# Kernel tuning notes

Hardware: AMD Instinct MI355X
Metric: run time of the kernel (lower is better)

The kernel has to match this reference:

```python
import jax, jax.numpy as jnp
import numpy as np

HEAD_SIZE = 64
NUM_HEADS = 8
D_MODEL = NUM_HEADS * HEAD_SIZE  # 512
B, T = 8, 1024
LN_EPS = 1e-3  # tf.keras LayerNormalization default epsilon


def setup_inputs() -> dict:
    key = jax.random.key(0)
    ks = jax.random.split(key, 10)
    s = 0.02
    return {
        "inputs": jax.random.normal(ks[0], (B, T, D_MODEL), jnp.float32),
        "pos": jax.random.normal(ks[1], (B, T, D_MODEL), jnp.float32),
        "gamma": jnp.ones((D_MODEL,), jnp.float32),
        "beta": jnp.zeros((D_MODEL,), jnp.float32),
        "query_kernel": jax.random.normal(ks[2], (NUM_HEADS, D_MODEL, HEAD_SIZE), jnp.float32) * s,
        "key_kernel": jax.random.normal(ks[3], (NUM_HEADS, D_MODEL, HEAD_SIZE), jnp.float32) * s,
        "value_kernel": jax.random.normal(ks[4], (NUM_HEADS, D_MODEL, HEAD_SIZE), jnp.float32) * s,
        "pos_kernel": jax.random.normal(ks[5], (NUM_HEADS, D_MODEL, HEAD_SIZE), jnp.float32) * s,
        "pos_bias_u": jax.random.normal(ks[6], (NUM_HEADS, HEAD_SIZE), jnp.float32) * s,
        "pos_bias_v": jax.random.normal(ks[7], (NUM_HEADS, HEAD_SIZE), jnp.float32) * s,
        "projection_kernel": jax.random.normal(ks[8], (NUM_HEADS, HEAD_SIZE, D_MODEL), jnp.float32) * s,
        "projection_bias": jnp.zeros((D_MODEL,), jnp.float32),
    }


def _layer_norm(x, gamma, beta):
    mean = jnp.mean(x, axis=-1, keepdims=True)
    var = jnp.mean(jnp.square(x - mean), axis=-1, keepdims=True)
    return (x - mean) * jax.lax.rsqrt(var + LN_EPS) * gamma + beta


def _relative_shift(x):
    # Transformer-XL shift trick: x is [B, H, N, M]
    b, h, n, m = x.shape
    x = jnp.pad(x, ((0, 0), (0, 0), (0, 0), (1, 0)))  # [B,H,N,M+1]
    x = x.reshape(b, h, m + 1, n)
    return x[:, :, 1:, :].reshape(b, h, n, m)


def reference(inputs, pos, gamma, beta, query_kernel, key_kernel, value_kernel,
              pos_kernel, pos_bias_u, pos_bias_v, projection_kernel, projection_bias):
    x = _layer_norm(inputs, gamma, beta)
    # per-head projections: [B,N,I] x [H,I,O] -> [B,N,H,O]
    q = jnp.einsum("bni,hio->bnho", x, query_kernel)
    k = jnp.einsum("bni,hio->bnho", x, key_kernel)
    v = jnp.einsum("bni,hio->bnho", x, value_kernel)
    p = jnp.einsum("bmi,hio->bmho", pos, pos_kernel)
    # content and position scores (Transformer-XL / Conformer relmha)
    matrix_ac = jnp.einsum("bnho,bmho->bhnm", q + pos_bias_u, k)
    matrix_bd = _relative_shift(jnp.einsum("bnho,bmho->bhnm", q + pos_bias_v, p))
    scores = (matrix_ac + matrix_bd) / jnp.sqrt(jnp.asarray(HEAD_SIZE, x.dtype))
    attn = jax.nn.softmax(scores, axis=-1)
    out = jnp.einsum("bhnm,bmho->bnho", attn, v)
    out = jnp.einsum("bnho,hoi->bni", out, projection_kernel) + projection_bias
    # dropout_prob=0 / inference -> identity; residual add
    return inputs + out
```

## Files before the change

kernel.cpp:

```cpp
#include <hip/hip_runtime.h>

#define BB 8
#define TT 1024
#define DD 512
#define HH 8
#define HS 64

typedef __attribute__((ext_vector_type(8))) short short8;
typedef __attribute__((ext_vector_type(4))) float f32x4;
typedef __attribute__((ext_vector_type(16))) float f32x16;

#if __has_builtin(__builtin_amdgcn_exp2f)
#define EXP2(x) __builtin_amdgcn_exp2f(x)
#else
#define EXP2(x) exp2f(x)
#endif

__device__ __forceinline__ float bf2f(unsigned short u) {
  union { unsigned int i; float f; } v; v.i = ((unsigned int)u) << 16; return v.f;
}
__device__ __forceinline__ unsigned short f2bf(float f) {
  union { float f; unsigned int i; } v; v.f = f;
  unsigned int i = v.i;
  return (unsigned short)((i + 0x7FFFu + ((i >> 16) & 1u)) >> 16);
}
__device__ __forceinline__ unsigned int cvt_pk_bf16(float lo, float hi) {
  unsigned int r;
  asm volatile("v_cvt_pk_bf16_f32 %0, %1, %2" : "=v"(r) : "v"(lo), "v"(hi));
  return r;
}

__device__ __forceinline__ size_t x16(int r, int k) {
  return (size_t)(r >> 4) * 8192 + ((k >> 5) * 512) + (((k >> 3) & 3) * 128) + ((r & 15) * 8) + (k & 7);
}
__device__ __forceinline__ size_t t32_addr(int n, int k) {
  return (size_t)(n >> 5) * 2048 + ((k >> 4) * 512) + (((k >> 3) & 1) * 256) + ((n & 31) * 8) + (k & 7);
}
__device__ __forceinline__ size_t vt_addr(int o, int m) {
  int s15 = (m & 3) | ((m & 4) << 1) | ((m & 8) >> 1);
  return (size_t)(m >> 5) * 2048 + (((m >> 4) & 1) * 1024) + ((o >> 5) * 512) +
         (((s15 >> 3) & 1) * 256) + ((o & 31) * 8) + (s15 & 7);
}

__global__ __launch_bounds__(256) void prep(const float* __restrict__ in,
                                            const float* __restrict__ pos,
                                            const float* __restrict__ gamma,
                                            const float* __restrict__ beta,
                                            const float* __restrict__ Wq, const float* __restrict__ Wk,
                                            const float* __restrict__ Wv, const float* __restrict__ Wp,
                                            const float* __restrict__ Wo,
                                            unsigned short* __restrict__ x,
                                            unsigned short* __restrict__ p16,
                                            unsigned short* __restrict__ Tq, unsigned short* __restrict__ Tk,
                                            unsigned short* __restrict__ Tv, unsigned short* __restrict__ Tp,
                                            unsigned short* __restrict__ Two) {
  int t = threadIdx.x;
  if (blockIdx.y == 2) {
    int g = blockIdx.x;
    if (g >= 40) return;
    int sel = g >> 3, gg = g & 7;
    if (sel < 4) {
      const float* win = sel == 0 ? Wq : sel == 1 ? Wk : sel == 2 ? Wv : Wp;
      unsigned short* wout = sel == 0 ? Tq : sel == 1 ? Tk : sel == 2 ? Tv : Tp;
      for (int idx = t; idx < 32768; idx += 256) {
        int of = idx >> 13, kk = (idx >> 9) & 15, l4 = (idx >> 7) & 3, l15 = (idx >> 3) & 15, e = idx & 7;
        int o = of * 16 + l15, k = kk * 32 + l4 * 8 + e;
        wout[(size_t)gg * 32768 + idx] = f2bf(win[(size_t)gg * 32768 + k * 64 + o]);
      }
    } else {
      for (int idx = t; idx < 32768; idx += 256) {
        int of = idx >> 13, kk = (idx >> 9) & 15, l4 = (idx >> 7) & 3, l15 = (idx >> 3) & 15, e = idx & 7;
        int i = gg * 64 + of * 16 + l15, k = kk * 32 + l4 * 8 + e;
        Two[(size_t)gg * 32768 + idx] = f2bf(Wo[(size_t)k * 512 + i]);
      }
    }
    return;
  }
  int rt = blockIdx.x;
  int ri = t >> 4, ki = t & 15;
  if (blockIdx.y == 0) {
    const float* rp = in + ((size_t)rt * 16 + ri) * DD + ki * 32;
    float v[32];
#pragma unroll
    for (int j = 0; j < 8; ++j) *(float4*)&v[j * 4] = *(const float4*)(rp + j * 4);
    float s = 0.f;
#pragma unroll
    for (int j = 0; j < 32; ++j) s += v[j];
    s += __shfl_xor(s, 1); s += __shfl_xor(s, 2); s += __shfl_xor(s, 4); s += __shfl_xor(s, 8);
    float mean = s * (1.0f / DD);
    float vs = 0.f;
#pragma unroll
    for (int j = 0; j < 32; ++j) { float d = v[j] - mean; vs += d * d; }
    vs += __shfl_xor(vs, 1); vs += __shfl_xor(vs, 2); vs += __shfl_xor(vs, 4); vs += __shfl_xor(vs, 8);
    float inv = rsqrtf(vs * (1.0f / DD) + 1e-3f);
    size_t base = (size_t)rt * 8192 + ki * 512 + ri * 8;
#pragma unroll
    for (int qg = 0; qg < 4; ++qg) {
      short8 u;
#pragma unroll
      for (int e = 0; e < 8; ++e) {
        int col = ki * 32 + qg * 8 + e;
        u[e] = (short)f2bf((v[qg * 8 + e] - mean) * inv * gamma[col] + beta[col]);
      }
      *(short8*)(x + base + qg * 128) = u;
    }
  } else {
    const float* rp = pos + ((size_t)rt * 16 + ri) * DD + ki * 32;
    size_t base = (size_t)rt * 8192 + ki * 512 + ri * 8;
#pragma unroll
    for (int qg = 0; qg < 4; ++qg) {
      float4 a = *(const float4*)(rp + qg * 8);
      float4 b = *(const float4*)(rp + qg * 8 + 4);
      short8 u;
      u[0] = (short)f2bf(a.x); u[1] = (short)f2bf(a.y); u[2] = (short)f2bf(a.z); u[3] = (short)f2bf(a.w);
      u[4] = (short)f2bf(b.x); u[5] = (short)f2bf(b.y); u[6] = (short)f2bf(b.z); u[7] = (short)f2bf(b.w);
      *(short8*)(p16 + base + qg * 128) = u;
    }
  }
}

#define MF16(a, b, c) __builtin_amdgcn_mfma_f32_16x16x32_bf16(a, b, c, 0, 0, 0)
#define MF32(a, b, c) __builtin_amdgcn_mfma_f32_32x32x16_bf16(a, b, c, 0, 0, 0)

__global__ __launch_bounds__(512) void proj2(const unsigned short* __restrict__ X,
                                             const unsigned short* __restrict__ POS,
                                             const unsigned short* __restrict__ Wtq,
                                             const unsigned short* __restrict__ Wtk,
                                             const unsigned short* __restrict__ Wtv,
                                             const unsigned short* __restrict__ Wtp,
                                             const float* __restrict__ bu,
                                             const float* __restrict__ bv,
                                             unsigned short* __restrict__ QU,
                                             unsigned short* __restrict__ QV,
                                             unsigned short* __restrict__ KT,
                                             unsigned short* __restrict__ VT,
                                             unsigned short* __restrict__ PT) {
  __shared__ __align__(16) unsigned short Wlds[32768];
  int tid = threadIdx.x;
  int w = tid >> 6, l = tid & 63;
  int l15 = l & 15, l4 = l >> 4;
  int rb = blockIdx.x, h = blockIdx.y, sel = blockIdx.z;
  const unsigned short* Wsrc = (sel == 0 ? Wtq : sel == 1 ? Wtk : sel == 2 ? Wtv : Wtp) + (size_t)h * 32768;
  const unsigned short* A = (sel == 3) ? POS : X;
#pragma unroll
  for (int i = 0; i < 8; ++i)
    *(short8*)(Wlds + (tid + i * 512) * 8) = *(const short8*)(Wsrc + (tid + i * 512) * 8);
  __syncthreads();

  int rt0 = rb * 32 + w * 4;
  f32x4 acc[4][4];
#pragma unroll
  for (int j4 = 0; j4 < 4; ++j4)
#pragma unroll
    for (int of = 0; of < 4; ++of) acc[j4][of] = (f32x4){0.f, 0.f, 0.f, 0.f};
  for (int kk = 0; kk < 16; ++kk) {
    short8 a0 = *(const short8*)(A + (size_t)(rt0 + 0) * 8192 + kk * 512 + l * 8);
    short8 a1 = *(const short8*)(A + (size_t)(rt0 + 1) * 8192 + kk * 512 + l * 8);
    short8 a2 = *(const short8*)(A + (size_t)(rt0 + 2) * 8192 + kk * 512 + l * 8);
    short8 a3 = *(const short8*)(A + (size_t)(rt0 + 3) * 8192 + kk * 512 + l * 8);
    const unsigned short* wp = Wlds + kk * 512 + l * 8;
    short8 w0 = *(const short8*)(wp);
    short8 w1 = *(const short8*)(wp + 8192);
    short8 w2 = *(const short8*)(wp + 16384);
    short8 w3 = *(const short8*)(wp + 24576);
    acc[0][0] = MF16(a0, w0, acc[0][0]); acc[0][1] = MF16(a0, w1, acc[0][1]);
    acc[0][2] = MF16(a0, w2, acc[0][2]); acc[0][3] = MF16(a0, w3, acc[0][3]);
    acc[1][0] = MF16(a1, w0, acc[1][0]); acc[1][1] = MF16(a1, w1, acc[1][1]);
    acc[1][2] = MF16(a1, w2, acc[1][2]); acc[1][3] = MF16(a1, w3, acc[1][3]);
    acc[2][0] = MF16(a2, w0, acc[2][0]); acc[2][1] = MF16(a2, w1, acc[2][1]);
    acc[2][2] = MF16(a2, w2, acc[2][2]); acc[2][3] = MF16(a2, w3, acc[2][3]);
    acc[3][0] = MF16(a3, w0, acc[3][0]); acc[3][1] = MF16(a3, w1, acc[3][1]);
    acc[3][2] = MF16(a3, w2, acc[3][2]); acc[3][3] = MF16(a3, w3, acc[3][3]);
  }

  if (sel == 0) {
    const float S = 0.125f * 1.44269504088896f;
#pragma unroll
    for (int of = 0; of < 4; ++of) {
      int o = of * 16 + l15;
      float bum = bu[h * HS + o], bvm = bv[h * HS + o];
#pragma unroll
      for (int j4 = 0; j4 < 4; ++j4)
#pragma unroll
        for (int j = 0; j < 4; ++j) {
          int r = (rt0 + j4) * 16 + l4 * 4 + j;
          int b = r >> 10, n = r & 1023;
          size_t bho = ((size_t)b * HH + h) * 65536;
          size_t ta = t32_addr(n, o);
          QU[bho + ta] = f2bf((acc[j4][of][j] + bum) * S);
          QV[bho + ta] = f2bf((acc[j4][of][j] + bvm) * S);
        }
    }
  } else if (sel == 1) {
#pragma unroll
    for (int of = 0; of < 4; ++of) {
      int o = of * 16 + l15;
#pragma unroll
      for (int j4 = 0; j4 < 4; ++j4)
#pragma unroll
        for (int j = 0; j < 4; ++j) {
          int r = (rt0 + j4) * 16 + l4 * 4 + j;
          int b = r >> 10, n = r & 1023;
          KT[((size_t)b * HH + h) * 65536 + t32_addr(n, o)] = f2bf(acc[j4][of][j]);
        }
    }
  } else if (sel == 2) {
#pragma unroll
    for (int of = 0; of < 4; ++of) {
      int o = of * 16 + l15;
#pragma unroll
      for (int j4 = 0; j4 < 4; ++j4)
#pragma unroll
        for (int j = 0; j < 4; ++j) {
          int r = (rt0 + j4) * 16 + l4 * 4 + j;
          int b = r >> 10, m = r & 1023;
          VT[((size_t)b * HH + h) * 65536 + vt_addr(o, m)] = f2bf(acc[j4][of][j]);
        }
    }
  } else {
#pragma unroll
    for (int of = 0; of < 4; ++of) {
      int o = of * 16 + l15;
#pragma unroll
      for (int j4 = 0; j4 < 4; ++j4)
#pragma unroll
        for (int j = 0; j < 4; ++j) {
          int r = (rt0 + j4) * 16 + l4 * 4 + j;
          int b = r >> 10, n = r & 1023;
          PT[((size_t)b * HH + h) * 65536 + t32_addr(n, o)] = f2bf(acc[j4][of][j]);
        }
    }
  }
}

__global__ __launch_bounds__(512) void out2(const unsigned short* __restrict__ A,
                                            const unsigned short* __restrict__ WoTT,
                                            const float* __restrict__ resid,
                                            const float* __restrict__ bias,
                                            float* __restrict__ Out) {
  __shared__ __align__(16) unsigned short Wlds[32768];
  int tid = threadIdx.x;
  int w = tid >> 6, l = tid & 63;
  int l15 = l & 15, l4 = l >> 4;
  int rb = blockIdx.x, cb = blockIdx.y;
  const unsigned short* Wsrc = WoTT + (size_t)cb * 32768;
#pragma unroll
  for (int i = 0; i < 8; ++i)
    *(short8*)(Wlds + (tid + i * 512) * 8) = *(const short8*)(Wsrc + (tid + i * 512) * 8);
  __syncthreads();

  int rt0 = rb * 32 + w * 4;
  f32x4 acc[4][4];
#pragma unroll
  for (int j4 = 0; j4 < 4; ++j4)
#pragma unroll
    for (int of = 0; of < 4; ++of) acc[j4][of] = (f32x4){0.f, 0.f, 0.f, 0.f};
  for (int kk = 0; kk < 16; ++kk) {
    short8 a0 = *(const short8*)(A + (size_t)(rt0 + 0) * 8192 + kk * 512 + l * 8);
    short8 a1 = *(const short8*)(A + (size_t)(rt0 + 1) * 8192 + kk * 512 + l * 8);
    short8 a2 = *(const short8*)(A + (size_t)(rt0 + 2) * 8192 + kk * 512 + l * 8);
    short8 a3 = *(const short8*)(A + (size_t)(rt0 + 3) * 8192 + kk * 512 + l * 8);
    const unsigned short* wp = Wlds + kk * 512 + l * 8;
    short8 w0 = *(const short8*)(wp);
    short8 w1 = *(const short8*)(wp + 8192);
    short8 w2 = *(const short8*)(wp + 16384);
    short8 w3 = *(const short8*)(wp + 24576);
    acc[0][0] = MF16(a0, w0, acc[0][0]); acc[0][1] = MF16(a0, w1, acc[0][1]);
    acc[0][2] = MF16(a0, w2, acc[0][2]); acc[0][3] = MF16(a0, w3, acc[0][3]);
    acc[1][0] = MF16(a1, w0, acc[1][0]); acc[1][1] = MF16(a1, w1, acc[1][1]);
    acc[1][2] = MF16(a1, w2, acc[1][2]); acc[1][3] = MF16(a1, w3, acc[1][3]);
    acc[2][0] = MF16(a2, w0, acc[2][0]); acc[2][1] = MF16(a2, w1, acc[2][1]);
    acc[2][2] = MF16(a2, w2, acc[2][2]); acc[2][3] = MF16(a2, w3, acc[2][3]);
    acc[3][0] = MF16(a3, w0, acc[3][0]); acc[3][1] = MF16(a3, w1, acc[3][1]);
    acc[3][2] = MF16(a3, w2, acc[3][2]); acc[3][3] = MF16(a3, w3, acc[3][3]);
  }
#pragma unroll
  for (int of = 0; of < 4; ++of) {
    int i = cb * 64 + of * 16 + l15;
    float bi = bias[i];
#pragma unroll
    for (int j4 = 0; j4 < 4; ++j4)
#pragma unroll
      for (int j = 0; j < 4; ++j) {
        int r = (rt0 + j4) * 16 + l4 * 4 + j;
        Out[(size_t)r * DD + i] = acc[j4][of][j] + bi + resid[(size_t)r * DD + i];
      }
  }
}

#define WLS 1036
__global__ __launch_bounds__(512, 4) void attn_mfma(const unsigned short* __restrict__ QT,
                                                    const unsigned short* __restrict__ QVT,
                                                    const unsigned short* __restrict__ KT,
                                                    const unsigned short* __restrict__ VT,
                                                    const unsigned short* __restrict__ PT,
                                                    unsigned short* __restrict__ pre) {
  int i = blockIdx.x;
  int slot = i >> 3;
  int p = (i & 7) * 8 + (slot >> 5);
  int nb = slot & 31;
  int b = p >> 3, h = p & 7;
  int n0 = nb * 32;
  __shared__ __align__(16) unsigned short Wl[34][WLS];
  int tid = threadIdx.x;
  int w = tid >> 6, l = tid & 63;
  int l31 = l & 31, hi = l >> 5;
  size_t bh = ((size_t)b * HH + h) * 65536;
  const unsigned short* QTb = QT  + bh;
  const unsigned short* QVb = QVT + bh;
  const unsigned short* KTb = KT  + bh;
  const unsigned short* PTb = PT  + bh;
  const unsigned short* VTb = VT  + bh;

  if (tid < 32) {
    int m = n0 + tid + 1;
    if (m <= TT - 1) Wl[tid][m] = 0;
  }
  {
    const unsigned short* aq = QVb + (size_t)nb * 2048 + l * 8;
    short8 a0 = *(const short8*)(aq);
    short8 a1 = *(const short8*)(aq + 512);
    short8 a2 = *(const short8*)(aq + 1024);
    short8 a3 = *(const short8*)(aq + 1536);
#pragma unroll
    for (int cg = 0; cg < 4; ++cg) {
      int ct = w + 8 * cg;
      const unsigned short* bp = PTb + (size_t)ct * 2048 + l * 8;
      f32x16 acc = {};
      acc = MF32(a0, *(const short8*)(bp),        acc);
      acc = MF32(a1, *(const short8*)(bp + 512),  acc);
      acc = MF32(a2, *(const short8*)(bp + 1024), acc);
      acc = MF32(a3, *(const short8*)(bp + 1536), acc);
      int c = ct * 32 + l31;
#pragma unroll
      for (int i2 = 0; i2 < 16; ++i2) {
        int rr = (i2 & 3) + 8 * (i2 >> 2) + 4 * hi;
        unsigned short v = f2bf(acc[i2]);
        int m1 = c + n0 + rr - (TT - 1);
        if (m1 >= 0) Wl[rr][m1] = v;
        int m2 = c + n0 + rr + 1;
        if (rr >= 1 && m2 <= TT - 1) Wl[rr - 1][m2] = v;
      }
    }
  }
  if (n0 + 32 < TT) {
    const unsigned short* aq = QVb + (size_t)(nb + 1) * 2048 + l * 8;
    short8 a0 = *(const short8*)(aq);
    short8 a1 = *(const short8*)(aq + 512);
    short8 a2 = *(const short8*)(aq + 1024);
    short8 a3 = *(const short8*)(aq + 1536);
    for (int ct = w; ct * 32 <= 990 - n0; ct += 8) {
      const unsigned short* bp = PTb + (size_t)ct * 2048 + l * 8;
      f32x16 acc = {};
      acc = MF32(a0, *(const short8*)(bp),        acc);
      acc = MF32(a1, *(const short8*)(bp + 512),  acc);
      acc = MF32(a2, *(const short8*)(bp + 1024), acc);
      acc = MF32(a3, *(const short8*)(bp + 1536), acc);
      if (hi == 0) {
        int m2 = ct * 32 + l31 + n0 + 33;
        if (m2 <= TT - 1) Wl[31][m2] = f2bf(acc[0]);
      }
    }
  }
  __syncthreads();

  const unsigned short* qtb = QTb + (size_t)nb * 2048 + l * 8;
  short8 qb0 = *(const short8*)(qtb);
  short8 qb1 = *(const short8*)(qtb + 512);
  short8 qb2 = *(const short8*)(qtb + 1024);
  short8 qb3 = *(const short8*)(qtb + 1536);
  f32x16 Oa0 = {}, Oa1 = {};
  float run_l = 0.f;

  short8 kc0, kc1, kc2, kc3;
  {
    const unsigned short* ktb = KTb + (size_t)w * 2048 + l * 8;
    kc0 = *(const short8*)(ktb);
    kc1 = *(const short8*)(ktb + 512);
    kc2 = *(const short8*)(ktb + 1024);
    kc3 = *(const short8*)(ktb + 1536);
  }

#pragma unroll 1
  for (int ci = 0; ci < 4; ++ci) {
    int mt = ci * 8 + w;
    int m0 = mt * 32;
    const unsigned short* vtb = VTb + (size_t)mt * 2048 + l * 8;
    short8 vv0 = *(const short8*)(vtb);
    short8 vv1 = *(const short8*)(vtb + 1024);
    short8 vv2 = *(const short8*)(vtb + 512);
    short8 vv3 = *(const short8*)(vtb + 1536);
    f32x16 s;
#pragma unroll
    for (int g = 0; g < 4; ++g) {
      ushort4 bd4 = *(const ushort4*)&Wl[l31][m0 + 8 * g + 4 * hi];
      s[4 * g + 0] = bf2f(bd4.x);
      s[4 * g + 1] = bf2f(bd4.y);
      s[4 * g + 2] = bf2f(bd4.z);
      s[4 * g + 3] = bf2f(bd4.w);
    }
    s = MF32(kc0, qb0, s);
    s = MF32(kc1, qb1, s);
    s = MF32(kc2, qb2, s);
    s = MF32(kc3, qb3, s);
    if (ci < 3) {
      const unsigned short* kn = KTb + (size_t)(mt + 8) * 2048 + l * 8;
      kc0 = *(const short8*)(kn);
      kc1 = *(const short8*)(kn + 512);
      kc2 = *(const short8*)(kn + 1024);
      kc3 = *(const short8*)(kn + 1536);
    }
    float sum = 0.f;
#pragma unroll
    for (int i2 = 0; i2 < 16; ++i2) { s[i2] = EXP2(s[i2]); sum += s[i2]; }
    sum += __shfl_xor(sum, 32);
    run_l += sum;
    short8 bp0, bp1;
    {
      unsigned int* u = (unsigned int*)&bp0;
      u[0] = cvt_pk_bf16(s[0], s[1]);
      u[1] = cvt_pk_bf16(s[2], s[3]);
      u[2] = cvt_pk_bf16(s[4], s[5]);
      u[3] = cvt_pk_bf16(s[6], s[7]);
      unsigned int* v2 = (unsigned int*)&bp1;
      v2[0] = cvt_pk_bf16(s[8], s[9]);
      v2[1] = cvt_pk_bf16(s[10], s[11]);
      v2[2] = cvt_pk_bf16(s[12], s[13]);
      v2[3] = cvt_pk_bf16(s[14], s[15]);
    }
    Oa0 = MF32(vv0, bp0, Oa0);
    Oa0 = MF32(vv1, bp1, Oa0);
    Oa1 = MF32(vv2, bp0, Oa1);
    Oa1 = MF32(vv3, bp1, Oa1);
  }

  __syncthreads();
  float* WLf = (float*)&Wl[0][0];
  float* myO = WLf + w * 2176;
#pragma unroll
  for (int i2 = 0; i2 < 16; ++i2) {
    int o0 = (i2 & 3) + 8 * (i2 >> 2) + 4 * hi;
    myO[o0 * 33 + l31]        = Oa0[i2];
    myO[(o0 + 32) * 33 + l31] = Oa1[i2];
  }
  if (l < 32) myO[2112 + l] = run_l;
  __syncthreads();
#pragma unroll
  for (int q4 = 0; q4 < 4; ++q4) {
    int q = w * 4 + q4;
    float denom = 0.f, val = 0.f;
#pragma unroll
    for (int w2 = 0; w2 < 8; ++w2) {
      denom += WLf[w2 * 2176 + 2112 + q];
      val   += WLf[w2 * 2176 + l * 33 + q];
    }
    pre[x16(b * TT + n0 + q, h * HS + l)] = f2bf(val / denom);
  }
}

extern "C" void kernel_launch(void* const* d_in, const int* in_sizes, int n_in,
                              void* d_out, int out_size, void* d_ws, size_t ws_size,
                              hipStream_t stream) {
  const float* inputs = (const float*)d_in[0];
  const float* pos    = (const float*)d_in[1];
  const float* gamma  = (const float*)d_in[2];
  const float* beta   = (const float*)d_in[3];
  const float* Wq = (const float*)d_in[4];
  const float* Wk = (const float*)d_in[5];
  const float* Wv = (const float*)d_in[6];
  const float* Wp = (const float*)d_in[7];
  const float* bu = (const float*)d_in[8];
  const float* bv = (const float*)d_in[9];
  const float* Wo = (const float*)d_in[10];
  const float* bo = (const float*)d_in[11];
  float* out = (float*)d_out;
  unsigned short* w16 = (unsigned short*)d_ws;

  const size_t T2 = (size_t)BB * TT * DD;
  unsigned short* x_bf  = w16;
  unsigned short* pre_b = x_bf  + T2;
  unsigned short* QUp   = pre_b + T2;
  unsigned short* QVp   = QUp   + T2;
  unsigned short* Kp    = QVp   + T2;
  unsigned short* Vtp   = Kp    + T2;
  unsigned short* Pp    = Vtp   + T2;
  unsigned short* Pos16 = Pp    + T2;
  unsigned short* WtQ   = Pos16 + T2;
  unsigned short* WtK   = WtQ + 262144;
  unsigned short* WtV   = WtK + 262144;
  unsigned short* WtP   = WtV + 262144;
  unsigned short* WoTT  = WtP + 262144;

  prep<<<dim3(512, 3), dim3(256), 0, stream>>>(inputs, pos, gamma, beta, Wq, Wk, Wv, Wp, Wo,
                                               x_bf, Pos16, WtQ, WtK, WtV, WtP, WoTT);
  proj2<<<dim3(16, 8, 4), dim3(512), 0, stream>>>(x_bf, Pos16, WtQ, WtK, WtV, WtP, bu, bv,
                                                  QUp, QVp, Kp, Vtp, Pp);
  attn_mfma<<<dim3(2048), dim3(512), 0, stream>>>(QUp, QVp, Kp, Vtp, Pp, pre_b);
  out2<<<dim3(16, 8), dim3(512), 0, stream>>>(pre_b, WoTT, inputs, bo, out);
}
```

Measured before the change: 153.0 us.

## Remap projection grids to 1D, prefetch V tiles, add MFMA priority hints

The proj2 and out2 grids become 1D, with the head or column block as the fastest-varying index, so that neighbouring blocks share weight slices and interleave differently across CUs. In the attention kernel, V tiles are now prefetched one iteration ahead, like the K tiles, using double-buffered registers. The MFMA sequences are wrapped in s_setprio so matrix work gets scheduling priority among waves. The prefetch raises register pressure, which may reduce occupancy.

```diff
diff --git a/kernel.cpp b/kernel.cpp
--- a/kernel.cpp
+++ b/kernel.cpp
@@ -139,7 +139,10 @@
   int tid = threadIdx.x;
   int w = tid >> 6, l = tid & 63;
   int l15 = l & 15, l4 = l >> 4;
-  int rb = blockIdx.x, h = blockIdx.y, sel = blockIdx.z;
+  int bi2 = blockIdx.x;
+  int h = bi2 & 7;
+  int t2 = bi2 >> 3;
+  int sel = t2 >> 4, rb = t2 & 15;
   const unsigned short* Wsrc = (sel == 0 ? Wtq : sel == 1 ? Wtk : sel == 2 ? Wtv : Wtp) + (size_t)h * 32768;
   const unsigned short* A = (sel == 3) ? POS : X;
 #pragma unroll
@@ -242,7 +245,7 @@
   int tid = threadIdx.x;
   int w = tid >> 6, l = tid & 63;
   int l15 = l & 15, l4 = l >> 4;
-  int rb = blockIdx.x, cb = blockIdx.y;
+  int cb = blockIdx.x & 7, rb = blockIdx.x >> 3;
   const unsigned short* Wsrc = WoTT + (size_t)cb * 32768;
 #pragma unroll
   for (int i = 0; i < 8; ++i)
@@ -327,10 +330,12 @@
       int ct = w + 8 * cg;
       const unsigned short* bp = PTb + (size_t)ct * 2048 + l * 8;
       f32x16 acc = {};
+      __builtin_amdgcn_s_setprio(1);
       acc = MF32(a0, *(const short8*)(bp),        acc);
       acc = MF32(a1, *(const short8*)(bp + 512),  acc);
       acc = MF32(a2, *(const short8*)(bp + 1024), acc);
       acc = MF32(a3, *(const short8*)(bp + 1536), acc);
+      __builtin_amdgcn_s_setprio(0);
       int c = ct * 32 + l31;
 #pragma unroll
       for (int i2 = 0; i2 < 16; ++i2) {
@@ -372,24 +377,24 @@
   f32x16 Oa0 = {}, Oa1 = {};
   float run_l = 0.f;
 
-  short8 kc0, kc1, kc2, kc3;
+  short8 kc0, kc1, kc2, kc3, vc0, vc1, vc2, vc3;
   {
     const unsigned short* ktb = KTb + (size_t)w * 2048 + l * 8;
     kc0 = *(const short8*)(ktb);
     kc1 = *(const short8*)(ktb + 512);
     kc2 = *(const short8*)(ktb + 1024);
     kc3 = *(const short8*)(ktb + 1536);
+    const unsigned short* vtb = VTb + (size_t)w * 2048 + l * 8;
+    vc0 = *(const short8*)(vtb);
+    vc1 = *(const short8*)(vtb + 1024);
+    vc2 = *(const short8*)(vtb + 512);
+    vc3 = *(const short8*)(vtb + 1536);
   }
 
 #pragma unroll 1
   for (int ci = 0; ci < 4; ++ci) {
     int mt = ci * 8 + w;
     int m0 = mt * 32;
-    const unsigned short* vtb = VTb + (size_t)mt * 2048 + l * 8;
-    short8 vv0 = *(const short8*)(vtb);
-    short8 vv1 = *(const short8*)(vtb + 1024);
-    short8 vv2 = *(const short8*)(vtb + 512);
-    short8 vv3 = *(const short8*)(vtb + 1536);
     f32x16 s;
 #pragma unroll
     for (int g = 0; g < 4; ++g) {
@@ -399,16 +404,24 @@
       s[4 * g + 2] = bf2f(bd4.z);
       s[4 * g + 3] = bf2f(bd4.w);
     }
+    __builtin_amdgcn_s_setprio(1);
     s = MF32(kc0, qb0, s);
     s = MF32(kc1, qb1, s);
     s = MF32(kc2, qb2, s);
     s = MF32(kc3, qb3, s);
+    __builtin_amdgcn_s_setprio(0);
+    short8 kn0, kn1, kn2, kn3, vn0, vn1, vn2, vn3;
     if (ci < 3) {
       const unsigned short* kn = KTb + (size_t)(mt + 8) * 2048 + l * 8;
-      kc0 = *(const short8*)(kn);
-      kc1 = *(const short8*)(kn + 512);
-      kc2 = *(const short8*)(kn + 1024);
-      kc3 = *(const short8*)(kn + 1536);
+      kn0 = *(const short8*)(kn);
+      kn1 = *(const short8*)(kn + 512);
+      kn2 = *(const short8*)(kn + 1024);
+      kn3 = *(const short8*)(kn + 1536);
+      const unsigned short* vn = VTb + (size_t)(mt + 8) * 2048 + l * 8;
+      vn0 = *(const short8*)(vn);
+      vn1 = *(const short8*)(vn + 1024);
+      vn2 = *(const short8*)(vn + 512);
+      vn3 = *(const short8*)(vn + 1536);
     }
     float sum = 0.f;
 #pragma unroll
@@ -428,10 +441,16 @@
       v2[2] = cvt_pk_bf16(s[12], s[13]);
       v2[3] = cvt_pk_bf16(s[14], s[15]);
     }
-    Oa0 = MF32(vv0, bp0, Oa0);
-    Oa0 = MF32(vv1, bp1, Oa0);
-    Oa1 = MF32(vv2, bp0, Oa1);
-    Oa1 = MF32(vv3, bp1, Oa1);
+    __builtin_amdgcn_s_setprio(1);
+    Oa0 = MF32(vc0, bp0, Oa0);
+    Oa0 = MF32(vc1, bp1, Oa0);
+    Oa1 = MF32(vc2, bp0, Oa1);
+    Oa1 = MF32(vc3, bp1, Oa1);
+    __builtin_amdgcn_s_setprio(0);
+    if (ci < 3) {
+      kc0 = kn0; kc1 = kn1; kc2 = kn2; kc3 = kn3;
+      vc0 = vn0; vc1 = vn1; vc2 = vn2; vc3 = vn3;
+    }
   }
 
   __syncthreads();
@@ -493,8 +512,8 @@
 
   prep<<<dim3(512, 3), dim3(256), 0, stream>>>(inputs, pos, gamma, beta, Wq, Wk, Wv, Wp, Wo,
                                                x_bf, Pos16, WtQ, WtK, WtV, WtP, WoTT);
-  proj2<<<dim3(16, 8, 4), dim3(512), 0, stream>>>(x_bf, Pos16, WtQ, WtK, WtV, WtP, bu, bv,
-                                                  QUp, QVp, Kp, Vtp, Pp);
+  proj2<<<dim3(512), dim3(512), 0, stream>>>(x_bf, Pos16, WtQ, WtK, WtV, WtP, bu, bv,
+                                             QUp, QVp, Kp, Vtp, Pp);
   attn_mfma<<<dim3(2048), dim3(512), 0, stream>>>(QUp, QVp, Kp, Vtp, Pp, pre_b);
-  out2<<<dim3(16, 8), dim3(512), 0, stream>>>(pre_b, WoTT, inputs, bo, out);
-}
+  out2<<<dim3(128), dim3(512), 0, stream>>>(pre_b, WoTT, inputs, bo, out);
+}
```

After: 195.8 us. 1.28x slower.
